# Optimization experiments

Measured on AMD Instinct MI355X. Metric: run time of the kernel, lower is better.

## Reference

```python
import jax, jax.numpy as jnp
import numpy as np
from jax import lax

B, C, H, W = 8, 256, 64, 64
E, K, OUT = 9, 3, 256
EPS = 1e-5


def setup_inputs() -> dict:
    key = jax.random.key(0)
    ks = jax.random.split(key, 12)
    return {
        "x": jax.random.normal(ks[0], (B, C, H, W), jnp.float32),
        "w_experts": jax.random.normal(ks[1], (E, C, K, K), jnp.float32) * 0.1,  # depthwise kernels (O=C, I=1 folded)
        "bn_gamma": jax.random.normal(ks[2], (E, C), jnp.float32) * 0.1 + 1.0,
        "bn_beta": jax.random.normal(ks[3], (E, C), jnp.float32) * 0.1,
        "bn_mean": jax.random.normal(ks[4], (E, C), jnp.float32) * 0.1,
        "bn_var": jax.random.uniform(ks[5], (E, C), jnp.float32, 0.5, 1.5),
        "scales": jnp.full((E, C), 0.1, jnp.float32),
        "w_out": jax.random.normal(ks[6], (OUT, C), jnp.float32) * (1.0 / np.sqrt(C)),  # 1x1 conv weight
        "out_gamma": jax.random.normal(ks[7], (OUT,), jnp.float32) * 0.1 + 1.0,
        "out_beta": jax.random.normal(ks[8], (OUT,), jnp.float32) * 0.1,
        "out_mean": jax.random.normal(ks[9], (OUT,), jnp.float32) * 0.1,
        "out_var": jax.random.uniform(ks[10], (OUT,), jnp.float32, 0.5, 1.5),
    }


def reference(x, w_experts, bn_gamma, bn_beta, bn_mean, bn_var, scales,
              w_out, out_gamma, out_beta, out_mean, out_var):
    # All E depthwise convs in ONE grouped conv: groups=C, E outputs per group.
    # kernel (E,C,K,K) -> (C,E,K,K) -> (C*E, 1, K, K); output group c holds experts of channel c.
    k = jnp.transpose(w_experts, (1, 0, 2, 3)).reshape(C * E, 1, K, K)
    y = lax.conv_general_dilated(
        x, k, window_strides=(1, 1), padding="SAME",
        feature_group_count=C,
        dimension_numbers=("NCHW", "OIHW", "NCHW"),
    )  # [B, C*E, H, W]
    y = y.reshape(x.shape[0], C, E, H, W)

    # Fold BN (eval-mode, running stats) and per-expert channel scale, then sum over experts.
    t = bn_gamma * lax.rsqrt(bn_var + EPS)          # [E, C]
    eff_scale = t * scales                          # [E, C]
    eff_bias = ((bn_beta - bn_mean * t) * scales).sum(0)  # [C]
    moe = jnp.einsum("bcehw,ec->bchw", y, eff_scale) + eff_bias[None, :, None, None]
    moe = jax.nn.silu(moe)

    # out_prj: 1x1 conv + BN + SiLU
    out = jnp.einsum("bchw,oc->bohw", moe, w_out)
    t2 = out_gamma * lax.rsqrt(out_var + EPS)       # [OUT]
    out = out * t2[None, :, None, None] + (out_beta - out_mean * t2)[None, :, None, None]
    return jax.nn.silu(out)
```

## Files before the change

kernel.cpp:

```cpp
#include <hip/hip_runtime.h>

#define EPS 1e-5f

typedef __attribute__((ext_vector_type(8))) __bf16 bf16x8;
typedef __attribute__((ext_vector_type(4))) float f32x4;

__device__ __forceinline__ float silu_f(float v) {
  return v / (1.f + __expf(-v));
}

__global__ __launch_bounds__(256) void prep_kernel(
    const float* __restrict__ w_experts, const float* __restrict__ bn_gamma,
    const float* __restrict__ bn_beta, const float* __restrict__ bn_mean,
    const float* __restrict__ bn_var, const float* __restrict__ scales,
    const float* __restrict__ w_out, const float* __restrict__ out_gamma,
    const float* __restrict__ out_beta, const float* __restrict__ out_mean,
    const float* __restrict__ out_var,
    float* __restrict__ eff_kernel, float* __restrict__ eff_bias,
    __bf16* __restrict__ w_eff, float* __restrict__ bias2)
{
  const int t = threadIdx.x;
  if (blockIdx.x == 0) {
    const int c = t;
    float k9[9];
#pragma unroll
    for (int r = 0; r < 9; ++r) k9[r] = 0.f;
    float bias = 0.f;
    for (int e = 0; e < 9; ++e) {
      const int ec = e * 256 + c;
      const float tt = bn_gamma[ec] * rsqrtf(bn_var[ec] + EPS);
      const float sc = scales[ec];
      const float es = tt * sc;
      bias += (bn_beta[ec] - bn_mean[ec] * tt) * sc;
      const float* wp = w_experts + (size_t)ec * 9;
#pragma unroll
      for (int r = 0; r < 9; ++r) k9[r] += es * wp[r];
    }
#pragma unroll
    for (int r = 0; r < 9; ++r) eff_kernel[c * 9 + r] = k9[r];
    eff_bias[c] = bias;
    const float t2 = out_gamma[c] * rsqrtf(out_var[c] + EPS);
    bias2[c] = out_beta[c] - out_mean[c] * t2;
  } else {
    const int i = (blockIdx.x - 1) * 256 + t;
    const int o = i >> 8;
    const float t2 = out_gamma[o] * rsqrtf(out_var[o] + EPS);
    w_eff[i] = (__bf16)(w_out[i] * t2);
  }
}

__global__ __launch_bounds__(512, 4) void fused_kernel(
    const float* __restrict__ x, const float* __restrict__ eff_kernel,
    const float* __restrict__ eff_bias, const __bf16* __restrict__ w_eff,
    const float* __restrict__ bias2, float* __restrict__ out)
{
  __shared__ __align__(16) __bf16 B_lds[64 * 264];
  __shared__ float kern_s[256 * 9];
  __shared__ float bias_s[256];
  const int t = threadIdx.x;
  const int id = blockIdx.x;
  const int b = id & 7;
  const int h = id >> 3;

  for (int i = t; i < 2304; i += 512) kern_s[i] = eff_kernel[i];
  if (t < 256) bias_s[t] = eff_bias[t];
  __syncthreads();

  const int lane = t & 63;
  const int wv = t >> 6;
  const int lg = lane >> 4;
  const int wq = lane & 15;
  const int w4 = wq * 4;
  const bool up_ok = (h > 0), dn_ok = (h < 63);

#pragma unroll
  for (int cg = 0; cg < 2; ++cg) {
#pragma unroll
    for (int cc4 = 0; cc4 < 4; ++cc4) {
      const int ch = cg * 128 + wv * 16 + cc4 * 4 + lg;
      const float* xc = x + (size_t)(b * 256 + ch) * 4096;

      float4 v0, v1, v2;
      v1 = *(const float4*)(xc + h * 64 + w4);
      if (up_ok) v0 = *(const float4*)(xc + (h - 1) * 64 + w4);
      else       v0 = make_float4(0.f, 0.f, 0.f, 0.f);
      if (dn_ok) v2 = *(const float4*)(xc + (h + 1) * 64 + w4);
      else       v2 = make_float4(0.f, 0.f, 0.f, 0.f);

      float k[9];
#pragma unroll
      for (int j = 0; j < 9; ++j) k[j] = kern_s[ch * 9 + j];
      const float bias = bias_s[ch];

      float rowv[3][6];
      const float4 vv[3] = {v0, v1, v2};
#pragma unroll
      for (int r = 0; r < 3; ++r) {
        float vl = __shfl_up(vv[r].w, 1);
        float vr = __shfl_down(vv[r].x, 1);
        rowv[r][0] = (wq == 0) ? 0.f : vl;
        rowv[r][1] = vv[r].x;
        rowv[r][2] = vv[r].y;
        rowv[r][3] = vv[r].z;
        rowv[r][4] = vv[r].w;
        rowv[r][5] = (wq == 15) ? 0.f : vr;
      }

#pragma unroll
      for (int j = 0; j < 4; ++j) {
        float s = bias;
#pragma unroll
        for (int r = 0; r < 3; ++r)
          s += k[r * 3] * rowv[r][j] + k[r * 3 + 1] * rowv[r][j + 1] + k[r * 3 + 2] * rowv[r][j + 2];
        B_lds[(w4 + j) * 264 + ch] = (__bf16)silu_f(s);
      }
    }
  }
  __syncthreads();

  const int quad = lg, l15 = wq;
  const int wave_o = wv * 32;

  f32x4 acc[2][4];
#pragma unroll
  for (int i = 0; i < 2; ++i)
#pragma unroll
    for (int j = 0; j < 4; ++j) acc[i][j] = (f32x4){0.f, 0.f, 0.f, 0.f};

#pragma unroll
  for (int kk = 0; kk < 8; ++kk) {
    bf16x8 af[2], bf[4];
#pragma unroll
    for (int i = 0; i < 2; ++i)
      af[i] = *(const bf16x8*)&w_eff[(size_t)(wave_o + i * 16 + l15) * 256 + kk * 32 + quad * 8];
#pragma unroll
    for (int j = 0; j < 4; ++j)
      bf[j] = *(const bf16x8*)&B_lds[(j * 16 + l15) * 264 + kk * 32 + quad * 8];
#pragma unroll
    for (int i = 0; i < 2; ++i)
#pragma unroll
      for (int j = 0; j < 4; ++j)
        acc[i][j] = __builtin_amdgcn_mfma_f32_16x16x32_bf16(af[i], bf[j], acc[i][j], 0, 0, 0);
  }

  float* outb = out + (size_t)b * 256 * 4096 + h * 64;
#pragma unroll
  for (int i = 0; i < 2; ++i) {
#pragma unroll
    for (int r = 0; r < 4; ++r) {
      const int o = wave_o + i * 16 + quad * 4 + r;
      const float bo = bias2[o];
#pragma unroll
      for (int j = 0; j < 4; ++j) {
        const int p = j * 16 + l15;
        outb[(size_t)o * 4096 + p] = silu_f(acc[i][j][r] + bo);
      }
    }
  }
}

extern "C" void kernel_launch(void* const* d_in, const int* in_sizes, int n_in,
                              void* d_out, int out_size, void* d_ws, size_t ws_size,
                              hipStream_t stream) {
  const float* x         = (const float*)d_in[0];
  const float* w_experts = (const float*)d_in[1];
  const float* bn_gamma  = (const float*)d_in[2];
  const float* bn_beta   = (const float*)d_in[3];
  const float* bn_mean   = (const float*)d_in[4];
  const float* bn_var    = (const float*)d_in[5];
  const float* scales    = (const float*)d_in[6];
  const float* w_out     = (const float*)d_in[7];
  const float* out_gamma = (const float*)d_in[8];
  const float* out_beta  = (const float*)d_in[9];
  const float* out_mean  = (const float*)d_in[10];
  const float* out_var   = (const float*)d_in[11];
  float* out = (float*)d_out;

  char* ws = (char*)d_ws;
  float* eff_kernel = (float*)(ws);
  float* eff_bias   = (float*)(ws + 9216);
  __bf16* w_eff     = (__bf16*)(ws + 10240);
  float* bias2      = (float*)(ws + 141312);

  hipLaunchKernelGGL(prep_kernel, dim3(257), dim3(256), 0, stream,
                     w_experts, bn_gamma, bn_beta, bn_mean, bn_var, scales,
                     w_out, out_gamma, out_beta, out_mean, out_var,
                     eff_kernel, eff_bias, w_eff, bias2);
  hipLaunchKernelGGL(fused_kernel, dim3(512), dim3(512), 0, stream,
                     x, eff_kernel, eff_bias, w_eff, bias2, out);
}
```

Measured before the change: 125.0 us.

## Process two rows per block and overlap depthwise stages with MFMA GEMM

Each block now handles two output rows with 1024 threads, so the halo rows of x are shared and fewer blocks launch. The depthwise conv is split into four channel chunks, and the later chunks' loads and compute are interleaved with the first GEMM k-steps, overlapping memory latency with MFMA work. The kernel weights and bias are packed into a 12-float stride so they can be read with vector LDS loads. The costs are more LDS per block and fewer blocks (256) in flight, which may hurt occupancy.

```diff
diff --git a/kernel.cpp b/kernel.cpp
--- a/kernel.cpp
+++ b/kernel.cpp
@@ -16,8 +16,8 @@
     const float* __restrict__ w_out, const float* __restrict__ out_gamma,
     const float* __restrict__ out_beta, const float* __restrict__ out_mean,
     const float* __restrict__ out_var,
-    float* __restrict__ eff_kernel, float* __restrict__ eff_bias,
-    __bf16* __restrict__ w_eff, float* __restrict__ bias2)
+    float* __restrict__ eff_kernel, __bf16* __restrict__ w_eff,
+    float* __restrict__ bias2)
 {
   const int t = threadIdx.x;
   if (blockIdx.x == 0) {
@@ -37,8 +37,10 @@
       for (int r = 0; r < 9; ++r) k9[r] += es * wp[r];
     }
 #pragma unroll
-    for (int r = 0; r < 9; ++r) eff_kernel[c * 9 + r] = k9[r];
-    eff_bias[c] = bias;
+    for (int r = 0; r < 9; ++r) eff_kernel[c * 12 + r] = k9[r];
+    eff_kernel[c * 12 + 9]  = bias;
+    eff_kernel[c * 12 + 10] = 0.f;
+    eff_kernel[c * 12 + 11] = 0.f;
     const float t2 = out_gamma[c] * rsqrtf(out_var[c] + EPS);
     bias2[c] = out_beta[c] - out_mean[c] * t2;
   } else {
@@ -49,77 +51,72 @@
   }
 }
 
-__global__ __launch_bounds__(512, 4) void fused_kernel(
+__global__ __launch_bounds__(1024, 4) void fused_kernel(
     const float* __restrict__ x, const float* __restrict__ eff_kernel,
-    const float* __restrict__ eff_bias, const __bf16* __restrict__ w_eff,
-    const float* __restrict__ bias2, float* __restrict__ out)
+    const __bf16* __restrict__ w_eff, const float* __restrict__ bias2,
+    float* __restrict__ out)
 {
-  __shared__ __align__(16) __bf16 B_lds[64 * 264];
-  __shared__ float kern_s[256 * 9];
-  __shared__ float bias_s[256];
+  __shared__ __align__(16) __bf16 B_lds[128 * 264];
+  __shared__ __align__(16) float kern_s[256 * 12];
+
   const int t = threadIdx.x;
   const int id = blockIdx.x;
   const int b = id & 7;
-  const int h = id >> 3;
-
-  for (int i = t; i < 2304; i += 512) kern_s[i] = eff_kernel[i];
-  if (t < 256) bias_s[t] = eff_bias[t];
-  __syncthreads();
+  const int h0 = (id >> 3) * 2;
+
+  for (int i = t; i < 3072; i += 1024) kern_s[i] = eff_kernel[i];
 
   const int lane = t & 63;
   const int wv = t >> 6;
   const int lg = lane >> 4;
   const int wq = lane & 15;
   const int w4 = wq * 4;
-  const bool up_ok = (h > 0), dn_ok = (h < 63);
-
-#pragma unroll
-  for (int cg = 0; cg < 2; ++cg) {
-#pragma unroll
-    for (int cc4 = 0; cc4 < 4; ++cc4) {
-      const int ch = cg * 128 + wv * 16 + cc4 * 4 + lg;
-      const float* xc = x + (size_t)(b * 256 + ch) * 4096;
-
-      float4 v0, v1, v2;
-      v1 = *(const float4*)(xc + h * 64 + w4);
-      if (up_ok) v0 = *(const float4*)(xc + (h - 1) * 64 + w4);
-      else       v0 = make_float4(0.f, 0.f, 0.f, 0.f);
-      if (dn_ok) v2 = *(const float4*)(xc + (h + 1) * 64 + w4);
-      else       v2 = make_float4(0.f, 0.f, 0.f, 0.f);
-
-      float k[9];
-#pragma unroll
-      for (int j = 0; j < 9; ++j) k[j] = kern_s[ch * 9 + j];
-      const float bias = bias_s[ch];
-
-      float rowv[3][6];
-      const float4 vv[3] = {v0, v1, v2};
-#pragma unroll
-      for (int r = 0; r < 3; ++r) {
-        float vl = __shfl_up(vv[r].w, 1);
-        float vr = __shfl_down(vv[r].x, 1);
-        rowv[r][0] = (wq == 0) ? 0.f : vl;
-        rowv[r][1] = vv[r].x;
-        rowv[r][2] = vv[r].y;
-        rowv[r][3] = vv[r].z;
-        rowv[r][4] = vv[r].w;
-        rowv[r][5] = (wq == 15) ? 0.f : vr;
+  const bool up_ok = (h0 > 0), dn_ok = (h0 < 62);
+  const float4 z4 = make_float4(0.f, 0.f, 0.f, 0.f);
+
+  auto dw_loads = [&](int it, float4* v) {
+    const int ch = it * 64 + wv * 4 + lg;
+    const float* xc = x + (size_t)(b * 256 + ch) * 4096 + w4;
+    v[1] = *(const float4*)(xc + h0 * 64);
+    v[2] = *(const float4*)(xc + (h0 + 1) * 64);
+    v[0] = up_ok ? *(const float4*)(xc + (h0 - 1) * 64) : z4;
+    v[3] = dn_ok ? *(const float4*)(xc + (h0 + 2) * 64) : z4;
+  };
+
+  auto dw_compute = [&](int it, const float4* v) {
+    const int ch = it * 64 + wv * 4 + lg;
+    const f32x4* kp = (const f32x4*)(kern_s + ch * 12);
+    const f32x4 ka = kp[0], kb = kp[1], kc = kp[2];
+    float rowv[4][6];
+#pragma unroll
+    for (int r = 0; r < 4; ++r) {
+      const float vl = __shfl_up(v[r].w, 1);
+      const float vr = __shfl_down(v[r].x, 1);
+      rowv[r][0] = (wq == 0) ? 0.f : vl;
+      rowv[r][1] = v[r].x; rowv[r][2] = v[r].y;
+      rowv[r][3] = v[r].z; rowv[r][4] = v[r].w;
+      rowv[r][5] = (wq == 15) ? 0.f : vr;
+    }
+    const float k0 = ka[0], k1 = ka[1], k2 = ka[2];
+    const float k3 = ka[3], k4 = kb[0], k5 = kb[1];
+    const float k6 = kb[2], k7 = kb[3], k8 = kc[0];
+    const float bias = kc[1];
+#pragma unroll
+    for (int rr = 0; rr < 2; ++rr) {
+#pragma unroll
+      for (int j = 0; j < 4; ++j) {
+        float s = bias
+          + k0 * rowv[rr][j]     + k1 * rowv[rr][j + 1]     + k2 * rowv[rr][j + 2]
+          + k3 * rowv[rr + 1][j] + k4 * rowv[rr + 1][j + 1] + k5 * rowv[rr + 1][j + 2]
+          + k6 * rowv[rr + 2][j] + k7 * rowv[rr + 2][j + 1] + k8 * rowv[rr + 2][j + 2];
+        B_lds[(rr * 64 + w4 + j) * 264 + ch] = (__bf16)silu_f(s);
       }
-
-#pragma unroll
-      for (int j = 0; j < 4; ++j) {
-        float s = bias;
-#pragma unroll
-        for (int r = 0; r < 3; ++r)
-          s += k[r * 3] * rowv[r][j] + k[r * 3 + 1] * rowv[r][j + 1] + k[r * 3 + 2] * rowv[r][j + 2];
-        B_lds[(w4 + j) * 264 + ch] = (__bf16)silu_f(s);
-      }
-    }
-  }
-  __syncthreads();
-
+    }
+  };
+
+  const int wrow   = wv >> 3;
+  const int wave_o = (wv & 7) * 32;
   const int quad = lg, l15 = wq;
-  const int wave_o = wv * 32;
 
   f32x4 acc[2][4];
 #pragma unroll
@@ -127,23 +124,36 @@
 #pragma unroll
     for (int j = 0; j < 4; ++j) acc[i][j] = (f32x4){0.f, 0.f, 0.f, 0.f};
 
-#pragma unroll
-  for (int kk = 0; kk < 8; ++kk) {
-    bf16x8 af[2], bf[4];
+  auto gemm_step = [&](int kk) {
+    bf16x8 af[2], bv[4];
 #pragma unroll
     for (int i = 0; i < 2; ++i)
       af[i] = *(const bf16x8*)&w_eff[(size_t)(wave_o + i * 16 + l15) * 256 + kk * 32 + quad * 8];
 #pragma unroll
     for (int j = 0; j < 4; ++j)
-      bf[j] = *(const bf16x8*)&B_lds[(j * 16 + l15) * 264 + kk * 32 + quad * 8];
+      bv[j] = *(const bf16x8*)&B_lds[(wrow * 64 + j * 16 + l15) * 264 + kk * 32 + quad * 8];
 #pragma unroll
     for (int i = 0; i < 2; ++i)
 #pragma unroll
       for (int j = 0; j < 4; ++j)
-        acc[i][j] = __builtin_amdgcn_mfma_f32_16x16x32_bf16(af[i], bf[j], acc[i][j], 0, 0, 0);
-  }
-
-  float* outb = out + (size_t)b * 256 * 4096 + h * 64;
+        acc[i][j] = __builtin_amdgcn_mfma_f32_16x16x32_bf16(af[i], bv[j], acc[i][j], 0, 0, 0);
+  };
+
+  float4 va[4], vb[4];
+  dw_loads(0, va); dw_loads(1, vb);
+  __syncthreads();
+  dw_compute(0, va); dw_compute(1, vb);
+  __syncthreads();
+  dw_loads(2, va);
+  gemm_step(0); gemm_step(1);
+  dw_compute(2, va);
+  dw_loads(3, vb);
+  gemm_step(2); gemm_step(3);
+  dw_compute(3, vb);
+  __syncthreads();
+  gemm_step(4); gemm_step(5); gemm_step(6); gemm_step(7);
+
+  float* outb = out + (size_t)(b * 256) * 4096 + (size_t)(h0 + wrow) * 64;
 #pragma unroll
   for (int i = 0; i < 2; ++i) {
 #pragma unroll
@@ -178,14 +188,13 @@
 
   char* ws = (char*)d_ws;
   float* eff_kernel = (float*)(ws);
-  float* eff_bias   = (float*)(ws + 9216);
-  __bf16* w_eff     = (__bf16*)(ws + 10240);
-  float* bias2      = (float*)(ws + 141312);
+  __bf16* w_eff     = (__bf16*)(ws + 12288);
+  float* bias2      = (float*)(ws + 143360);
 
   hipLaunchKernelGGL(prep_kernel, dim3(257), dim3(256), 0, stream,
                      w_experts, bn_gamma, bn_beta, bn_mean, bn_var, scales,
                      w_out, out_gamma, out_beta, out_mean, out_var,
-                     eff_kernel, eff_bias, w_eff, bias2);
-  hipLaunchKernelGGL(fused_kernel, dim3(512), dim3(512), 0, stream,
-                     x, eff_kernel, eff_bias, w_eff, bias2, out);
-}
+                     eff_kernel, w_eff, bias2);
+  hipLaunchKernelGGL(fused_kernel, dim3(256), dim3(1024), 0, stream,
+                     x, eff_kernel, w_eff, bias2, out);
+}
```

After: 127.0 us. Within noise of the previous version (+1.6%).
